# Optimization experiments

Measured on AMD Instinct MI355X. Metric: run time of the kernel, lower is better.

The kernel has to match this reference:

```python
import jax, jax.numpy as jnp
import numpy as np

N_NODES = 50000
N_EDGES = 800000
H = 128


def _mlp2(x, W1, b1, W2, b2):
    # Linear -> ReLU -> Linear
    h = jax.nn.relu(x @ W1 + b1)
    return h @ W2 + b2


def setup_inputs() -> dict:
    key = jax.random.key(0)
    ks = jax.random.split(key, 12)
    glorot = lambda k, fi, fo: jax.random.normal(k, (fi, fo), jnp.float32) * (1.0 / np.sqrt(fi))
    return {
        "x": jax.random.normal(ks[0], (N_NODES, H), jnp.float32),
        "edge_index": jax.random.randint(ks[1], (2, N_EDGES), 0, N_NODES, dtype=jnp.int64),
        "edge_attr": jax.random.normal(ks[2], (N_EDGES, H), jnp.float32),
        # edge MLP: 3H -> H -> H
        "We1": glorot(ks[3], 3 * H, H),
        "be1": jnp.zeros((H,), jnp.float32),
        "We2": glorot(ks[4], H, H),
        "be2": jnp.zeros((H,), jnp.float32),
        # node MLP: 2H -> H -> H
        "Wn1": glorot(ks[5], 2 * H, H),
        "bn1": jnp.zeros((H,), jnp.float32),
        "Wn2": glorot(ks[6], H, H),
        "bn2": jnp.zeros((H,), jnp.float32),
    }


def reference(x, edge_index, edge_attr, We1, be1, We2, be2, Wn1, bn1, Wn2, bn2):
    row, col = edge_index[0], edge_index[1]
    # gather + concat -> edge MLP  [E, 3H] -> [E, H]
    edge_inputs = jnp.concatenate([x[row], x[col], edge_attr], axis=-1)
    messages = _mlp2(edge_inputs, We1, be1, We2, be2)
    # scatter_add by destination node
    agg = jax.ops.segment_sum(messages, col, num_segments=x.shape[0])
    # concat -> node MLP  [N, 2H] -> [N, H]
    node_inputs = jnp.concatenate([x, agg], axis=-1)
    return _mlp2(node_inputs, Wn1, bn1, Wn2, bn2)
```

## Files before the change

### kernel.cpp

```cpp
#include <hip/hip_runtime.h>
#include <hip/hip_bf16.h>
#include <stdint.h>

#define N_NODES 50000
#define N_EDGES 800000
#define H 128

typedef short bf16x8 __attribute__((ext_vector_type(8)));
typedef float f32x4 __attribute__((ext_vector_type(4)));

__device__ __forceinline__ short f2bfs(float f) {
    __hip_bfloat16 h = __float2bfloat16(f);
    return *(short*)&h;
}

__device__ __forceinline__ bf16x8 cvt8(const float* __restrict__ p) {
    const float4* q = (const float4*)p;
    float4 a = q[0], b = q[1];
    bf16x8 r;
    r[0] = f2bfs(a.x); r[1] = f2bfs(a.y); r[2] = f2bfs(a.z); r[3] = f2bfs(a.w);
    r[4] = f2bfs(b.x); r[5] = f2bfs(b.y); r[6] = f2bfs(b.z); r[7] = f2bfs(b.w);
    return r;
}

__global__ void prep_weights(const float* __restrict__ We1, const float* __restrict__ We2,
                             const float* __restrict__ Wn1, const float* __restrict__ Wn2,
                             unsigned short* __restrict__ wb) {
    int i = blockIdx.x * 256 + threadIdx.x;
    if (i >= 114688) return;
    const float* W; int idx;
    if (i < 49152)      { W = We1; idx = i; }
    else if (i < 65536) { W = We2; idx = i - 49152; }
    else if (i < 98304) { W = Wn1; idx = i - 65536; }
    else                { W = Wn2; idx = i - 98304; }
    int f = idx >> 9, lane = (idx >> 3) & 63, j = idx & 7;
    int kt = f >> 3, nt = f & 7;
    int k = kt * 32 + (lane >> 4) * 8 + j;
    int n = nt * 16 + (lane & 15);
    wb[i] = (unsigned short)f2bfs(W[k * H + n]);
}

__global__ void prep_x(const float* __restrict__ x, unsigned short* __restrict__ xb) {
    int i = blockIdx.x * 256 + threadIdx.x;
    if (i >= (N_NODES * H) / 8) return;
    bf16x8 v = cvt8(x + (size_t)i * 8);
    *(bf16x8*)(xb + (size_t)i * 8) = v;
}

__global__ void hist_col(const int* __restrict__ ei, int* __restrict__ cnt) {
    int e = blockIdx.x * 256 + threadIdx.x;
    if (e < N_EDGES) atomicAdd(&cnt[ei[N_EDGES + e]], 1);
}

__global__ void scan_hist(const int* __restrict__ cnt, int* __restrict__ cursor) {
    __shared__ int wsum[16];
    __shared__ int stot;
    __shared__ int sbase_s;
    const int tid = threadIdx.x;
    const int lane = tid & 63, wid = tid >> 6;
    if (tid == 0) sbase_s = 0;
    __syncthreads();
    for (int base = 0; base < N_NODES; base += 1024) {
        int i = base + tid;
        int v = (i < N_NODES) ? cnt[i] : 0;
        int incl = v;
#pragma unroll
        for (int off = 1; off < 64; off <<= 1) {
            int t = __shfl_up(incl, off);
            if (lane >= off) incl += t;
        }
        if (lane == 63) wsum[wid] = incl;
        __syncthreads();
        if (wid == 0) {
            int wv = (lane < 16) ? wsum[lane] : 0;
            int winc = wv;
#pragma unroll
            for (int off = 1; off < 16; off <<= 1) {
                int t = __shfl_up(winc, off);
                if (lane >= off) winc += t;
            }
            if (lane < 16) wsum[lane] = winc - wv;
            if (lane == 15) stot = winc;
        }
        __syncthreads();
        if (i < N_NODES) cursor[i] = sbase_s + wsum[wid] + (incl - v);
        __syncthreads();
        if (tid == 0) sbase_s += stot;
        __syncthreads();
    }
}

__global__ void build_perm(const int* __restrict__ ei, int* __restrict__ cursor,
                           int* __restrict__ perm) {
    int e = blockIdx.x * 256 + threadIdx.x;
    if (e < N_EDGES) {
        int pos = atomicAdd(&cursor[ei[N_EDGES + e]], 1);
        perm[pos] = e;
    }
}

__launch_bounds__(256)
__global__ void edge_mlp(const unsigned short* __restrict__ xb,
                         const int* __restrict__ ei,
                         const float* __restrict__ ea,
                         const float* __restrict__ be1,
                         const float* __restrict__ be2,
                         const unsigned short* __restrict__ wb,
                         const int* __restrict__ perm,
                         float* __restrict__ agg) {
    __shared__ __align__(16) char smem[4][8192];
    const int tid = threadIdx.x;
    const int wave = tid >> 6, lane = tid & 63;
    const int c = lane & 15, quad = lane >> 4;
    const int e0 = (blockIdx.x * 4 + wave) * 32;

    short (*hb)[4][64][8] = (short (*)[4][64][8])smem[wave];
    float* msg = (float*)smem[wave];

    const bf16x8* __restrict__ BW1 = (const bf16x8*)wb;
    const bf16x8* __restrict__ BW2 = (const bf16x8*)(wb + 49152);

    float be1v[8], be2v[8];
#pragma unroll
    for (int nt = 0; nt < 8; ++nt) {
        be1v[nt] = be1[nt * 16 + c];
        be2v[nt] = be2[nt * 16 + c];
    }

    int myp = 0, myd = 0;
    if (lane < 32) { myp = perm[e0 + lane]; myd = ei[N_EDGES + myp]; }

    const unsigned short* pxb[2][2];
    const float* pea[2];
#pragma unroll
    for (int t = 0; t < 2; ++t) {
        int p_tc = __shfl(myp, t * 16 + c);
        int d_tc = __shfl(myd, t * 16 + c);
        int r_tc = ei[p_tc];
        pxb[t][0] = xb + (size_t)r_tc * H;
        pxb[t][1] = xb + (size_t)d_tc * H;
        pea[t]    = ea + (size_t)p_tc * H;
    }

    f32x4 acc[2][8];
#pragma unroll
    for (int t = 0; t < 2; ++t)
#pragma unroll
        for (int nt = 0; nt < 8; ++nt)
            acc[t][nt] = (f32x4){be1v[nt], be1v[nt], be1v[nt], be1v[nt]};

#pragma unroll
    for (int kt = 0; kt < 12; ++kt) {
        const int off = (kt & 3) * 32 + quad * 8;
        bf16x8 a0, a1;
        if (kt < 8) {
            a0 = *(const bf16x8*)(pxb[0][kt >> 2] + off);
            a1 = *(const bf16x8*)(pxb[1][kt >> 2] + off);
        } else {
            a0 = cvt8(pea[0] + off);
            a1 = cvt8(pea[1] + off);
        }
#pragma unroll
        for (int nt = 0; nt < 8; ++nt) {
            bf16x8 b = BW1[(kt * 8 + nt) * 64 + lane];
            acc[0][nt] = __builtin_amdgcn_mfma_f32_16x16x32_bf16(a0, b, acc[0][nt], 0, 0, 0);
            acc[1][nt] = __builtin_amdgcn_mfma_f32_16x16x32_bf16(a1, b, acc[1][nt], 0, 0, 0);
        }
    }

#pragma unroll
    for (int t = 0; t < 2; ++t)
#pragma unroll
        for (int nt = 0; nt < 8; ++nt) {
            int kt2 = nt >> 1;
            int laneq = 16 * ((nt * 2 + (c >> 3)) & 3);
#pragma unroll
            for (int r = 0; r < 4; ++r) {
                float v = acc[t][nt][r];
                v = v > 0.f ? v : 0.f;
                hb[t][kt2][quad * 4 + r + laneq][c & 7] = f2bfs(v);
            }
        }
    __syncthreads();

    f32x4 acc2[2][8];
#pragma unroll
    for (int t = 0; t < 2; ++t)
#pragma unroll
        for (int nt = 0; nt < 8; ++nt)
            acc2[t][nt] = (f32x4){be2v[nt], be2v[nt], be2v[nt], be2v[nt]};

#pragma unroll
    for (int kt = 0; kt < 4; ++kt) {
        bf16x8 a0 = *(const bf16x8*)&hb[0][kt][lane][0];
        bf16x8 a1 = *(const bf16x8*)&hb[1][kt][lane][0];
#pragma unroll
        for (int nt = 0; nt < 8; ++nt) {
            bf16x8 b = BW2[(kt * 8 + nt) * 64 + lane];
            acc2[0][nt] = __builtin_amdgcn_mfma_f32_16x16x32_bf16(a0, b, acc2[0][nt], 0, 0, 0);
            acc2[1][nt] = __builtin_amdgcn_mfma_f32_16x16x32_bf16(a1, b, acc2[1][nt], 0, 0, 0);
        }
    }
    __syncthreads();

#pragma unroll
    for (int t = 0; t < 2; ++t) {
#pragma unroll
        for (int nt = 0; nt < 8; ++nt)
#pragma unroll
            for (int r = 0; r < 4; ++r)
                msg[(quad * 4 + r) * 128 + ((nt * 16 + c) ^ (quad * 8))] = acc2[t][nt][r];
        __syncthreads();

        float s0 = 0.f, s1 = 0.f;
        int dprev = __builtin_amdgcn_readlane(myd, t * 16);
#pragma unroll
        for (int i = 0; i < 16; ++i) {
            int di = __builtin_amdgcn_readlane(myd, t * 16 + i);
            int idx = i * 128 + (lane ^ ((i >> 2) * 8));
            float v0 = msg[idx];
            float v1 = msg[idx + 64];
            if (i > 0 && di != dprev) {
                atomicAdd(agg + (size_t)dprev * H + lane, s0);
                atomicAdd(agg + (size_t)dprev * H + 64 + lane, s1);
                s0 = v0; s1 = v1; dprev = di;
            } else {
                s0 += v0; s1 += v1;
            }
        }
        atomicAdd(agg + (size_t)dprev * H + lane, s0);
        atomicAdd(agg + (size_t)dprev * H + 64 + lane, s1);
        __syncthreads();
    }
}

__launch_bounds__(128)
__global__ void node_mlp(const unsigned short* __restrict__ xb,
                         const float* __restrict__ agg,
                         const float* __restrict__ bn1,
                         const float* __restrict__ bn2,
                         const unsigned short* __restrict__ wb,
                         float* __restrict__ out) {
    __shared__ __align__(16) char smem[2][8192];
    const int tid = threadIdx.x;
    const int wave = tid >> 6, lane = tid & 63;
    const int c = lane & 15, quad = lane >> 4;
    const int v0 = (blockIdx.x * 2 + wave) * 32;
    short (*hb)[4][64][8] = (short (*)[4][64][8])smem[wave];

    const bf16x8* __restrict__ BN1 = (const bf16x8*)(wb + 65536);
    const bf16x8* __restrict__ BN2 = (const bf16x8*)(wb + 98304);

    float b1v[8], b2v[8];
#pragma unroll
    for (int nt = 0; nt < 8; ++nt) {
        b1v[nt] = bn1[nt * 16 + c];
        b2v[nt] = bn2[nt * 16 + c];
    }

    const unsigned short* pxb[2];
    const float* pag[2];
#pragma unroll
    for (int t = 0; t < 2; ++t) {
        int v = v0 + t * 16 + c;
        v = v < N_NODES ? v : N_NODES - 1;
        pxb[t] = xb  + (size_t)v * H;
        pag[t] = agg + (size_t)v * H;
    }

    f32x4 acc[2][8];
#pragma unroll
    for (int t = 0; t < 2; ++t)
#pragma unroll
        for (int nt = 0; nt < 8; ++nt)
            acc[t][nt] = (f32x4){b1v[nt], b1v[nt], b1v[nt], b1v[nt]};

#pragma unroll
    for (int kt = 0; kt < 8; ++kt) {
        const int off = (kt & 3) * 32 + quad * 8;
        bf16x8 a0, a1;
        if (kt < 4) {
            a0 = *(const bf16x8*)(pxb[0] + off);
            a1 = *(const bf16x8*)(pxb[1] + off);
        } else {
            a0 = cvt8(pag[0] + off);
            a1 = cvt8(pag[1] + off);
        }
#pragma unroll
        for (int nt = 0; nt < 8; ++nt) {
            bf16x8 b = BN1[(kt * 8 + nt) * 64 + lane];
            acc[0][nt] = __builtin_amdgcn_mfma_f32_16x16x32_bf16(a0, b, acc[0][nt], 0, 0, 0);
            acc[1][nt] = __builtin_amdgcn_mfma_f32_16x16x32_bf16(a1, b, acc[1][nt], 0, 0, 0);
        }
    }

#pragma unroll
    for (int t = 0; t < 2; ++t)
#pragma unroll
        for (int nt = 0; nt < 8; ++nt) {
            int kt2 = nt >> 1;
            int laneq = 16 * ((nt * 2 + (c >> 3)) & 3);
#pragma unroll
            for (int r = 0; r < 4; ++r) {
                float v = acc[t][nt][r];
                v = v > 0.f ? v : 0.f;
                hb[t][kt2][quad * 4 + r + laneq][c & 7] = f2bfs(v);
            }
        }
    __syncthreads();

    f32x4 acc2[2][8];
#pragma unroll
    for (int t = 0; t < 2; ++t)
#pragma unroll
        for (int nt = 0; nt < 8; ++nt)
            acc2[t][nt] = (f32x4){b2v[nt], b2v[nt], b2v[nt], b2v[nt]};

#pragma unroll
    for (int kt = 0; kt < 4; ++kt) {
        bf16x8 a0 = *(const bf16x8*)&hb[0][kt][lane][0];
        bf16x8 a1 = *(const bf16x8*)&hb[1][kt][lane][0];
#pragma unroll
        for (int nt = 0; nt < 8; ++nt) {
            bf16x8 b = BN2[(kt * 8 + nt) * 64 + lane];
            acc2[0][nt] = __builtin_amdgcn_mfma_f32_16x16x32_bf16(a0, b, acc2[0][nt], 0, 0, 0);
            acc2[1][nt] = __builtin_amdgcn_mfma_f32_16x16x32_bf16(a1, b, acc2[1][nt], 0, 0, 0);
        }
    }

#pragma unroll
    for (int t = 0; t < 2; ++t)
#pragma unroll
        for (int nt = 0; nt < 8; ++nt)
#pragma unroll
            for (int r = 0; r < 4; ++r) {
                int v = v0 + t * 16 + quad * 4 + r;
                if (v < N_NODES)
                    out[(size_t)v * H + nt * 16 + c] = acc2[t][nt][r];
            }
}

extern "C" void kernel_launch(void* const* d_in, const int* in_sizes, int n_in,
                              void* d_out, int out_size, void* d_ws, size_t ws_size,
                              hipStream_t stream) {
    const float* x   = (const float*)d_in[0];
    const int*   ei  = (const int*)d_in[1];
    const float* ea  = (const float*)d_in[2];
    const float* We1 = (const float*)d_in[3];
    const float* be1 = (const float*)d_in[4];
    const float* We2 = (const float*)d_in[5];
    const float* be2 = (const float*)d_in[6];
    const float* Wn1 = (const float*)d_in[7];
    const float* bn1 = (const float*)d_in[8];
    const float* Wn2 = (const float*)d_in[9];
    const float* bn2 = (const float*)d_in[10];
    float* out = (float*)d_out;

    char* base = (char*)d_ws;
    unsigned short* wb   = (unsigned short*)base;
    float*          agg  = (float*)(base + 262144);
    int*            cnt  = (int*)(base + 25862144);
    int*            cur  = (int*)(base + 26066944);
    int*            perm = (int*)(base + 26271744);
    unsigned short* xbuf = (unsigned short*)(base + 29471744);

    hipMemsetAsync(agg, 0, 25600000 + 204800, stream);
    prep_weights<<<448, 256, 0, stream>>>(We1, We2, Wn1, Wn2, wb);
    prep_x<<<3125, 256, 0, stream>>>(x, xbuf);
    hist_col<<<3125, 256, 0, stream>>>(ei, cnt);
    scan_hist<<<1, 1024, 0, stream>>>(cnt, cur);
    build_perm<<<3125, 256, 0, stream>>>(ei, cur, perm);
    edge_mlp<<<6250, 256, 0, stream>>>(xbuf, ei, ea, be1, be2, wb, perm, agg);
    node_mlp<<<782, 128, 0, stream>>>(xbuf, agg, bn1, bn2, wb, out);
}
```

Measured before the change: 1.215 ms.

## Restructure GNN via linearity: precompute node projections, fuse We2 into node MLP

Splits the first edge-MLP layer so the x[row] and x[col] projections are computed once per node (XW) rather than once per edge. Per edge only the edge_attr projection is computed, stored as bf16, and processed in chunks so it can stay cache-resident. Because the second edge layer is linear, it moves after the scatter-sum: We2 is folded into the agg half of Wn1, and be2 becomes a degree-scaled bias. This removes most per-edge matrix work at the cost of gathering fp32 per-node rows, extra kernel launches and more intermediate buffers.

```diff
diff --git a/kernel.cpp b/kernel.cpp
--- a/kernel.cpp
+++ b/kernel.cpp
@@ -5,6 +5,7 @@
 #define N_NODES 50000
 #define N_EDGES 800000
 #define H 128
+#define CHUNK 100000
 
 typedef short bf16x8 __attribute__((ext_vector_type(8)));
 typedef float f32x4 __attribute__((ext_vector_type(4)));
@@ -12,6 +13,9 @@
 __device__ __forceinline__ short f2bfs(float f) {
     __hip_bfloat16 h = __float2bfloat16(f);
     return *(short*)&h;
+}
+__device__ __forceinline__ float bfs2f(unsigned short u) {
+    return __uint_as_float(((unsigned int)u) << 16);
 }
 
 __device__ __forceinline__ bf16x8 cvt8(const float* __restrict__ p) {
@@ -23,28 +27,38 @@
     return r;
 }
 
-__global__ void prep_weights(const float* __restrict__ We1, const float* __restrict__ We2,
-                             const float* __restrict__ Wn1, const float* __restrict__ Wn2,
+__global__ void wfuse_c2(const float* __restrict__ We2, const float* __restrict__ Wn1,
+                         const float* __restrict__ be2,
+                         float* __restrict__ wfuse, float* __restrict__ c2) {
+    int k = blockIdx.x;
+    int n = threadIdx.x;
+    float s = 0.f;
+    if (k < 128) {
+        for (int m = 0; m < 128; ++m) s += We2[k * 128 + m] * Wn1[(128 + m) * 128 + n];
+        wfuse[k * 128 + n] = s;
+    } else {
+        for (int m = 0; m < 128; ++m) s += be2[m] * Wn1[(128 + m) * 128 + n];
+        c2[n] = s;
+    }
+}
+
+__global__ void prep_weights(const float* __restrict__ We1, const float* __restrict__ Wn1,
+                             const float* __restrict__ Wn2, const float* __restrict__ wfuse,
                              unsigned short* __restrict__ wb) {
     int i = blockIdx.x * 256 + threadIdx.x;
-    if (i >= 114688) return;
-    const float* W; int idx;
-    if (i < 49152)      { W = We1; idx = i; }
-    else if (i < 65536) { W = We2; idx = i - 49152; }
-    else if (i < 98304) { W = Wn1; idx = i - 65536; }
-    else                { W = Wn2; idx = i - 98304; }
+    if (i >= 98304) return;
+    const float* W; int idx; int which;
+    if (i < 49152)      { W = We1; idx = i; which = 0; }
+    else if (i < 81920) { W = Wn1; idx = i - 49152; which = 1; }
+    else                { W = Wn2; idx = i - 81920; which = 2; }
     int f = idx >> 9, lane = (idx >> 3) & 63, j = idx & 7;
     int kt = f >> 3, nt = f & 7;
     int k = kt * 32 + (lane >> 4) * 8 + j;
     int n = nt * 16 + (lane & 15);
-    wb[i] = (unsigned short)f2bfs(W[k * H + n]);
-}
-
-__global__ void prep_x(const float* __restrict__ x, unsigned short* __restrict__ xb) {
-    int i = blockIdx.x * 256 + threadIdx.x;
-    if (i >= (N_NODES * H) / 8) return;
-    bf16x8 v = cvt8(x + (size_t)i * 8);
-    *(bf16x8*)(xb + (size_t)i * 8) = v;
+    float v;
+    if (which == 1 && kt >= 4) v = wfuse[(k - 128) * 128 + n];
+    else                       v = W[k * H + n];
+    wb[i] = (unsigned short)f2bfs(v);
 }
 
 __global__ void hist_col(const int* __restrict__ ei, int* __restrict__ cnt) {
@@ -100,244 +114,180 @@
 }
 
 __launch_bounds__(256)
-__global__ void edge_mlp(const unsigned short* __restrict__ xb,
-                         const int* __restrict__ ei,
-                         const float* __restrict__ ea,
-                         const float* __restrict__ be1,
-                         const float* __restrict__ be2,
-                         const unsigned short* __restrict__ wb,
-                         const int* __restrict__ perm,
-                         float* __restrict__ agg) {
-    __shared__ __align__(16) char smem[4][8192];
-    const int tid = threadIdx.x;
-    const int wave = tid >> 6, lane = tid & 63;
-    const int c = lane & 15, quad = lane >> 4;
-    const int e0 = (blockIdx.x * 4 + wave) * 32;
-
-    short (*hb)[4][64][8] = (short (*)[4][64][8])smem[wave];
-    float* msg = (float*)smem[wave];
-
+__global__ void xw_gemm(const float* __restrict__ x, const unsigned short* __restrict__ wb,
+                        float* __restrict__ XW) {
+    int tidx = blockIdx.x * 4 + (threadIdx.x >> 6);
+    if (tidx >= 3125) return;
+    const int lane = threadIdx.x & 63, c = lane & 15, quad = lane >> 4;
     const bf16x8* __restrict__ BW1 = (const bf16x8*)wb;
-    const bf16x8* __restrict__ BW2 = (const bf16x8*)(wb + 49152);
-
-    float be1v[8], be2v[8];
-#pragma unroll
-    for (int nt = 0; nt < 8; ++nt) {
-        be1v[nt] = be1[nt * 16 + c];
-        be2v[nt] = be2[nt * 16 + c];
-    }
-
-    int myp = 0, myd = 0;
-    if (lane < 32) { myp = perm[e0 + lane]; myd = ei[N_EDGES + myp]; }
-
-    const unsigned short* pxb[2][2];
-    const float* pea[2];
-#pragma unroll
-    for (int t = 0; t < 2; ++t) {
-        int p_tc = __shfl(myp, t * 16 + c);
-        int d_tc = __shfl(myd, t * 16 + c);
-        int r_tc = ei[p_tc];
-        pxb[t][0] = xb + (size_t)r_tc * H;
-        pxb[t][1] = xb + (size_t)d_tc * H;
-        pea[t]    = ea + (size_t)p_tc * H;
-    }
-
-    f32x4 acc[2][8];
-#pragma unroll
-    for (int t = 0; t < 2; ++t)
-#pragma unroll
-        for (int nt = 0; nt < 8; ++nt)
-            acc[t][nt] = (f32x4){be1v[nt], be1v[nt], be1v[nt], be1v[nt]};
-
-#pragma unroll
-    for (int kt = 0; kt < 12; ++kt) {
-        const int off = (kt & 3) * 32 + quad * 8;
-        bf16x8 a0, a1;
-        if (kt < 8) {
-            a0 = *(const bf16x8*)(pxb[0][kt >> 2] + off);
-            a1 = *(const bf16x8*)(pxb[1][kt >> 2] + off);
+    const float* xr = x + (size_t)(tidx * 16 + c) * H;
+    f32x4 acc[16];
+#pragma unroll
+    for (int j = 0; j < 16; ++j) acc[j] = (f32x4){0.f, 0.f, 0.f, 0.f};
+#pragma unroll
+    for (int kt = 0; kt < 4; ++kt) {
+        bf16x8 a = cvt8(xr + kt * 32 + quad * 8);
+#pragma unroll
+        for (int j = 0; j < 16; ++j) {
+            int frag = (j < 8) ? (kt * 8 + j) : ((kt + 4) * 8 + j - 8);
+            bf16x8 b = BW1[frag * 64 + lane];
+            acc[j] = __builtin_amdgcn_mfma_f32_16x16x32_bf16(a, b, acc[j], 0, 0, 0);
+        }
+    }
+#pragma unroll
+    for (int j = 0; j < 16; ++j)
+#pragma unroll
+        for (int r = 0; r < 4; ++r)
+            XW[(size_t)(tidx * 16 + quad * 4 + r) * 256 + j * 16 + c] = acc[j][r];
+}
+
+__launch_bounds__(256)
+__global__ void ea_gemm(const float* __restrict__ ea, const int* __restrict__ perm,
+                        const float* __restrict__ be1, const unsigned short* __restrict__ wb,
+                        unsigned short* __restrict__ EW, int p0c) {
+    int w = blockIdx.x * 4 + (threadIdx.x >> 6);
+    if (w >= CHUNK / 16) return;
+    const int lane = threadIdx.x & 63, c = lane & 15, quad = lane >> 4;
+    const bf16x8* __restrict__ BW1 = (const bf16x8*)wb;
+    int e = perm[p0c + w * 16 + c];
+    const float* pea = ea + (size_t)e * H;
+    float be1v[8];
+#pragma unroll
+    for (int nt = 0; nt < 8; ++nt) be1v[nt] = be1[nt * 16 + c];
+    f32x4 acc[8];
+#pragma unroll
+    for (int nt = 0; nt < 8; ++nt)
+        acc[nt] = (f32x4){be1v[nt], be1v[nt], be1v[nt], be1v[nt]};
+#pragma unroll
+    for (int kt = 0; kt < 4; ++kt) {
+        bf16x8 a = cvt8(pea + kt * 32 + quad * 8);
+#pragma unroll
+        for (int nt = 0; nt < 8; ++nt) {
+            bf16x8 b = BW1[((kt + 8) * 8 + nt) * 64 + lane];
+            acc[nt] = __builtin_amdgcn_mfma_f32_16x16x32_bf16(a, b, acc[nt], 0, 0, 0);
+        }
+    }
+#pragma unroll
+    for (int nt = 0; nt < 8; ++nt)
+#pragma unroll
+        for (int r = 0; r < 4; ++r)
+            EW[(size_t)(w * 16 + quad * 4 + r) * H + nt * 16 + c] = (unsigned short)f2bfs(acc[nt][r]);
+}
+
+__launch_bounds__(256)
+__global__ void edge_gather(const int* __restrict__ ei, const int* __restrict__ perm,
+                            const unsigned short* __restrict__ EW, const float* __restrict__ XW,
+                            float* __restrict__ aggH, int p0c) {
+    int g = blockIdx.x * 4 + (threadIdx.x >> 6);
+    if (g >= CHUNK / 16) return;
+    const int lane = threadIdx.x & 63;
+    int myp = perm[p0c + g * 16 + (lane & 15)];
+    int myd = ei[N_EDGES + myp];
+    int myr = ei[myp];
+    const unsigned short* ewb = EW + (size_t)g * 16 * H;
+    float s0 = 0.f, s1 = 0.f;
+    int dprev = __builtin_amdgcn_readlane(myd, 0);
+#pragma unroll 4
+    for (int i = 0; i < 16; ++i) {
+        int di = __builtin_amdgcn_readlane(myd, i);
+        int ri = __builtin_amdgcn_readlane(myr, i);
+        const float* xa = XW + (size_t)ri * 256;
+        const float* xb = XW + (size_t)di * 256 + 128;
+        float v0 = bfs2f(ewb[i * H + lane])      + xa[lane]      + xb[lane];
+        float v1 = bfs2f(ewb[i * H + 64 + lane]) + xa[64 + lane] + xb[64 + lane];
+        v0 = v0 > 0.f ? v0 : 0.f;
+        v1 = v1 > 0.f ? v1 : 0.f;
+        if (i && di != dprev) {
+            atomicAdd(aggH + (size_t)dprev * H + lane, s0);
+            atomicAdd(aggH + (size_t)dprev * H + 64 + lane, s1);
+            s0 = v0; s1 = v1;
         } else {
-            a0 = cvt8(pea[0] + off);
-            a1 = cvt8(pea[1] + off);
-        }
-#pragma unroll
-        for (int nt = 0; nt < 8; ++nt) {
-            bf16x8 b = BW1[(kt * 8 + nt) * 64 + lane];
-            acc[0][nt] = __builtin_amdgcn_mfma_f32_16x16x32_bf16(a0, b, acc[0][nt], 0, 0, 0);
-            acc[1][nt] = __builtin_amdgcn_mfma_f32_16x16x32_bf16(a1, b, acc[1][nt], 0, 0, 0);
-        }
-    }
-
-#pragma unroll
-    for (int t = 0; t < 2; ++t)
-#pragma unroll
-        for (int nt = 0; nt < 8; ++nt) {
-            int kt2 = nt >> 1;
-            int laneq = 16 * ((nt * 2 + (c >> 3)) & 3);
-#pragma unroll
-            for (int r = 0; r < 4; ++r) {
-                float v = acc[t][nt][r];
-                v = v > 0.f ? v : 0.f;
-                hb[t][kt2][quad * 4 + r + laneq][c & 7] = f2bfs(v);
-            }
-        }
-    __syncthreads();
-
-    f32x4 acc2[2][8];
-#pragma unroll
-    for (int t = 0; t < 2; ++t)
-#pragma unroll
-        for (int nt = 0; nt < 8; ++nt)
-            acc2[t][nt] = (f32x4){be2v[nt], be2v[nt], be2v[nt], be2v[nt]};
-
-#pragma unroll
-    for (int kt = 0; kt < 4; ++kt) {
-        bf16x8 a0 = *(const bf16x8*)&hb[0][kt][lane][0];
-        bf16x8 a1 = *(const bf16x8*)&hb[1][kt][lane][0];
-#pragma unroll
-        for (int nt = 0; nt < 8; ++nt) {
-            bf16x8 b = BW2[(kt * 8 + nt) * 64 + lane];
-            acc2[0][nt] = __builtin_amdgcn_mfma_f32_16x16x32_bf16(a0, b, acc2[0][nt], 0, 0, 0);
-            acc2[1][nt] = __builtin_amdgcn_mfma_f32_16x16x32_bf16(a1, b, acc2[1][nt], 0, 0, 0);
-        }
-    }
-    __syncthreads();
-
-#pragma unroll
-    for (int t = 0; t < 2; ++t) {
-#pragma unroll
-        for (int nt = 0; nt < 8; ++nt)
-#pragma unroll
-            for (int r = 0; r < 4; ++r)
-                msg[(quad * 4 + r) * 128 + ((nt * 16 + c) ^ (quad * 8))] = acc2[t][nt][r];
-        __syncthreads();
-
-        float s0 = 0.f, s1 = 0.f;
-        int dprev = __builtin_amdgcn_readlane(myd, t * 16);
-#pragma unroll
-        for (int i = 0; i < 16; ++i) {
-            int di = __builtin_amdgcn_readlane(myd, t * 16 + i);
-            int idx = i * 128 + (lane ^ ((i >> 2) * 8));
-            float v0 = msg[idx];
-            float v1 = msg[idx + 64];
-            if (i > 0 && di != dprev) {
-                atomicAdd(agg + (size_t)dprev * H + lane, s0);
-                atomicAdd(agg + (size_t)dprev * H + 64 + lane, s1);
-                s0 = v0; s1 = v1; dprev = di;
-            } else {
-                s0 += v0; s1 += v1;
-            }
-        }
-        atomicAdd(agg + (size_t)dprev * H + lane, s0);
-        atomicAdd(agg + (size_t)dprev * H + 64 + lane, s1);
-        __syncthreads();
-    }
-}
-
-__launch_bounds__(128)
-__global__ void node_mlp(const unsigned short* __restrict__ xb,
-                         const float* __restrict__ agg,
-                         const float* __restrict__ bn1,
-                         const float* __restrict__ bn2,
-                         const unsigned short* __restrict__ wb,
-                         float* __restrict__ out) {
-    __shared__ __align__(16) char smem[2][8192];
-    const int tid = threadIdx.x;
-    const int wave = tid >> 6, lane = tid & 63;
-    const int c = lane & 15, quad = lane >> 4;
-    const int v0 = (blockIdx.x * 2 + wave) * 32;
-    short (*hb)[4][64][8] = (short (*)[4][64][8])smem[wave];
-
-    const bf16x8* __restrict__ BN1 = (const bf16x8*)(wb + 65536);
-    const bf16x8* __restrict__ BN2 = (const bf16x8*)(wb + 98304);
-
-    float b1v[8], b2v[8];
+            s0 += v0; s1 += v1;
+        }
+        dprev = di;
+    }
+    atomicAdd(aggH + (size_t)dprev * H + lane, s0);
+    atomicAdd(aggH + (size_t)dprev * H + 64 + lane, s1);
+}
+
+__launch_bounds__(256)
+__global__ void node1(const float* __restrict__ x, const float* __restrict__ aggH,
+                      const int* __restrict__ cnt, const float* __restrict__ bn1,
+                      const float* __restrict__ c2, const unsigned short* __restrict__ wb,
+                      unsigned short* __restrict__ Hn) {
+    int tidx = blockIdx.x * 4 + (threadIdx.x >> 6);
+    if (tidx >= 3125) return;
+    const int lane = threadIdx.x & 63, c = lane & 15, quad = lane >> 4;
+    const bf16x8* __restrict__ BN1 = (const bf16x8*)(wb + 49152);
+    const float* xr = x    + (size_t)(tidx * 16 + c) * H;
+    const float* ar = aggH + (size_t)(tidx * 16 + c) * H;
+    float b1v[8], c2v[8];
 #pragma unroll
     for (int nt = 0; nt < 8; ++nt) {
         b1v[nt] = bn1[nt * 16 + c];
-        b2v[nt] = bn2[nt * 16 + c];
-    }
-
-    const unsigned short* pxb[2];
-    const float* pag[2];
-#pragma unroll
-    for (int t = 0; t < 2; ++t) {
-        int v = v0 + t * 16 + c;
-        v = v < N_NODES ? v : N_NODES - 1;
-        pxb[t] = xb  + (size_t)v * H;
-        pag[t] = agg + (size_t)v * H;
-    }
-
-    f32x4 acc[2][8];
-#pragma unroll
-    for (int t = 0; t < 2; ++t)
-#pragma unroll
-        for (int nt = 0; nt < 8; ++nt)
-            acc[t][nt] = (f32x4){b1v[nt], b1v[nt], b1v[nt], b1v[nt]};
-
+        c2v[nt] = c2[nt * 16 + c];
+    }
+    float dg[4];
+#pragma unroll
+    for (int r = 0; r < 4; ++r) dg[r] = (float)cnt[tidx * 16 + quad * 4 + r];
+    f32x4 acc[8];
+#pragma unroll
+    for (int nt = 0; nt < 8; ++nt)
+#pragma unroll
+        for (int r = 0; r < 4; ++r)
+            acc[nt][r] = b1v[nt] + dg[r] * c2v[nt];
 #pragma unroll
     for (int kt = 0; kt < 8; ++kt) {
-        const int off = (kt & 3) * 32 + quad * 8;
-        bf16x8 a0, a1;
-        if (kt < 4) {
-            a0 = *(const bf16x8*)(pxb[0] + off);
-            a1 = *(const bf16x8*)(pxb[1] + off);
-        } else {
-            a0 = cvt8(pag[0] + off);
-            a1 = cvt8(pag[1] + off);
-        }
+        const float* src = (kt < 4) ? (xr + kt * 32) : (ar + (kt - 4) * 32);
+        bf16x8 a = cvt8(src + quad * 8);
 #pragma unroll
         for (int nt = 0; nt < 8; ++nt) {
             bf16x8 b = BN1[(kt * 8 + nt) * 64 + lane];
-            acc[0][nt] = __builtin_amdgcn_mfma_f32_16x16x32_bf16(a0, b, acc[0][nt], 0, 0, 0);
-            acc[1][nt] = __builtin_amdgcn_mfma_f32_16x16x32_bf16(a1, b, acc[1][nt], 0, 0, 0);
-        }
-    }
-
-#pragma unroll
-    for (int t = 0; t < 2; ++t)
+            acc[nt] = __builtin_amdgcn_mfma_f32_16x16x32_bf16(a, b, acc[nt], 0, 0, 0);
+        }
+    }
+#pragma unroll
+    for (int nt = 0; nt < 8; ++nt) {
+        int kt2 = nt >> 1;
+        int laneq = 16 * ((nt * 2 + (c >> 3)) & 3);
+#pragma unroll
+        for (int r = 0; r < 4; ++r) {
+            float v = acc[nt][r];
+            v = v > 0.f ? v : 0.f;
+            Hn[(size_t)((tidx * 4 + kt2) * 64 + quad * 4 + r + laneq) * 8 + (c & 7)] =
+                (unsigned short)f2bfs(v);
+        }
+    }
+}
+
+__launch_bounds__(256)
+__global__ void node2(const unsigned short* __restrict__ Hn, const float* __restrict__ bn2,
+                      const unsigned short* __restrict__ wb, float* __restrict__ out) {
+    int tidx = blockIdx.x * 4 + (threadIdx.x >> 6);
+    if (tidx >= 3125) return;
+    const int lane = threadIdx.x & 63, c = lane & 15, quad = lane >> 4;
+    const bf16x8* __restrict__ BN2 = (const bf16x8*)(wb + 81920);
+    float b2v[8];
+#pragma unroll
+    for (int nt = 0; nt < 8; ++nt) b2v[nt] = bn2[nt * 16 + c];
+    f32x4 acc[8];
+#pragma unroll
+    for (int nt = 0; nt < 8; ++nt)
+        acc[nt] = (f32x4){b2v[nt], b2v[nt], b2v[nt], b2v[nt]};
+#pragma unroll
+    for (int kt2 = 0; kt2 < 4; ++kt2) {
+        bf16x8 a = *(const bf16x8*)&Hn[(size_t)((tidx * 4 + kt2) * 64 + lane) * 8];
 #pragma unroll
         for (int nt = 0; nt < 8; ++nt) {
-            int kt2 = nt >> 1;
-            int laneq = 16 * ((nt * 2 + (c >> 3)) & 3);
-#pragma unroll
-            for (int r = 0; r < 4; ++r) {
-                float v = acc[t][nt][r];
-                v = v > 0.f ? v : 0.f;
-                hb[t][kt2][quad * 4 + r + laneq][c & 7] = f2bfs(v);
-            }
-        }
-    __syncthreads();
-
-    f32x4 acc2[2][8];
-#pragma unroll
-    for (int t = 0; t < 2; ++t)
-#pragma unroll
-        for (int nt = 0; nt < 8; ++nt)
-            acc2[t][nt] = (f32x4){b2v[nt], b2v[nt], b2v[nt], b2v[nt]};
-
-#pragma unroll
-    for (int kt = 0; kt < 4; ++kt) {
-        bf16x8 a0 = *(const bf16x8*)&hb[0][kt][lane][0];
-        bf16x8 a1 = *(const bf16x8*)&hb[1][kt][lane][0];
-#pragma unroll
-        for (int nt = 0; nt < 8; ++nt) {
-            bf16x8 b = BN2[(kt * 8 + nt) * 64 + lane];
-            acc2[0][nt] = __builtin_amdgcn_mfma_f32_16x16x32_bf16(a0, b, acc2[0][nt], 0, 0, 0);
-            acc2[1][nt] = __builtin_amdgcn_mfma_f32_16x16x32_bf16(a1, b, acc2[1][nt], 0, 0, 0);
-        }
-    }
-
-#pragma unroll
-    for (int t = 0; t < 2; ++t)
-#pragma unroll
-        for (int nt = 0; nt < 8; ++nt)
-#pragma unroll
-            for (int r = 0; r < 4; ++r) {
-                int v = v0 + t * 16 + quad * 4 + r;
-                if (v < N_NODES)
-                    out[(size_t)v * H + nt * 16 + c] = acc2[t][nt][r];
-            }
+            bf16x8 b = BN2[(kt2 * 8 + nt) * 64 + lane];
+            acc[nt] = __builtin_amdgcn_mfma_f32_16x16x32_bf16(a, b, acc[nt], 0, 0, 0);
+        }
+    }
+#pragma unroll
+    for (int nt = 0; nt < 8; ++nt)
+#pragma unroll
+        for (int r = 0; r < 4; ++r)
+            out[(size_t)(tidx * 16 + quad * 4 + r) * H + nt * 16 + c] = acc[nt][r];
 }
 
 extern "C" void kernel_launch(void* const* d_in, const int* in_sizes, int n_in,
@@ -357,19 +307,28 @@
     float* out = (float*)d_out;
 
     char* base = (char*)d_ws;
-    unsigned short* wb   = (unsigned short*)base;
-    float*          agg  = (float*)(base + 262144);
-    int*            cnt  = (int*)(base + 25862144);
-    int*            cur  = (int*)(base + 26066944);
-    int*            perm = (int*)(base + 26271744);
-    unsigned short* xbuf = (unsigned short*)(base + 29471744);
-
-    hipMemsetAsync(agg, 0, 25600000 + 204800, stream);
-    prep_weights<<<448, 256, 0, stream>>>(We1, We2, Wn1, Wn2, wb);
-    prep_x<<<3125, 256, 0, stream>>>(x, xbuf);
+    unsigned short* wb    = (unsigned short*)base;
+    float*          wfuse = (float*)(base + 262144);
+    float*          c2    = (float*)(base + 327680);
+    float*          aggH  = (float*)(base + 331776);
+    int*            cnt   = (int*)(base + 25931776);
+    int*            cur   = (int*)(base + 26131776);
+    int*            perm  = (int*)(base + 26331776);
+    float*          XW    = (float*)(base + 29531776);
+    unsigned short* EW    = (unsigned short*)(base + 80731776);
+    unsigned short* Hn    = EW;
+
+    hipMemsetAsync(aggH, 0, 25600000 + 200000, stream);
+    wfuse_c2<<<129, 128, 0, stream>>>(We2, Wn1, be2, wfuse, c2);
+    prep_weights<<<384, 256, 0, stream>>>(We1, Wn1, Wn2, wfuse, wb);
+    xw_gemm<<<782, 256, 0, stream>>>(x, wb, XW);
     hist_col<<<3125, 256, 0, stream>>>(ei, cnt);
     scan_hist<<<1, 1024, 0, stream>>>(cnt, cur);
     build_perm<<<3125, 256, 0, stream>>>(ei, cur, perm);
-    edge_mlp<<<6250, 256, 0, stream>>>(xbuf, ei, ea, be1, be2, wb, perm, agg);
-    node_mlp<<<782, 128, 0, stream>>>(xbuf, agg, bn1, bn2, wb, out);
-}
+    for (int cch = 0; cch < 8; ++cch) {
+        ea_gemm<<<1563, 256, 0, stream>>>(ea, perm, be1, wb, EW, cch * CHUNK);
+        edge_gather<<<1563, 256, 0, stream>>>(ei, perm, EW, XW, aggH, cch * CHUNK);
+    }
+    node1<<<782, 256, 0, stream>>>(x, aggH, cnt, bn1, c2, wb, Hn);
+    node2<<<782, 256, 0, stream>>>(Hn, bn2, wb, out);
+}
```

Measured after the change: 1.027 ms. 15.4% less time.
